# Kernel optimization log

Measured on AMD Instinct MI355X. Metric: run time of the kernel, lower is better.

Reference implementation:

```python
import jax, jax.numpy as jnp
import numpy as np

B, S, E, H, V, OOV = 128, 400, 512, 512, 50257, 50
VEXT = V + OOV


def setup_inputs() -> dict:
    key = jax.random.key(0)
    ks = jax.random.split(key, 20)
    w = lambda k, shp: (0.02 * jax.random.normal(k, shp)).astype(jnp.float32)
    return {
        'input_emb': jax.random.normal(ks[0], (B, 1, E), jnp.float32),
        'input_feed': jax.random.normal(ks[1], (B, 1, H), jnp.float32),
        'hidden': jax.random.normal(ks[2], (1, B, H), jnp.float32),
        'context': jax.random.normal(ks[3], (1, B, H), jnp.float32),
        'states': jax.random.normal(ks[4], (B, S, H), jnp.float32),
        'states_features': jax.random.normal(ks[5], (B, S, H), jnp.float32),
        'source_mask': jnp.ones((B, S), jnp.float32),
        'coverage': jnp.zeros((B, S), jnp.float32),
        'source_ids': jax.random.randint(ks[6], (B, S), 0, VEXT, jnp.int32),
        'W_ic': w(ks[7], (E, H + E)), 'b_ic': jnp.zeros((E,), jnp.float32),
        'W_ih': w(ks[8], (4 * H, E)), 'W_hh': w(ks[9], (4 * H, H)),
        'b_ih': jnp.zeros((4 * H,), jnp.float32), 'b_hh': jnp.zeros((4 * H,), jnp.float32),
        'W_dec': w(ks[10], (H, H)), 'b_att': jnp.zeros((H,), jnp.float32),
        'v_att': w(ks[11], (H,)), 'w_c': w(ks[12], (1,)),
        'W_out': w(ks[13], (H, 2 * H)), 'b_out': jnp.zeros((H,), jnp.float32),
        'W_pg': w(ks[14], (1, H)), 'b_pg': jnp.zeros((1,), jnp.float32),
        'W_v': w(ks[15], (V, H)), 'b_v': jnp.zeros((V,), jnp.float32),
    }


def reference(input_emb, input_feed, hidden, context, states, states_features,
              source_mask, coverage, source_ids,
              W_ic, b_ic, W_ih, W_hh, b_ih, b_hh,
              W_dec, b_att, v_att, w_c, W_out, b_out,
              W_pg, b_pg, W_v, b_v):
    # x = input_context(cat(input_emb, input_feed))  -> [B,1,E]
    x = jnp.concatenate([input_emb, input_feed], axis=2) @ W_ic.T + b_ic
    # single LSTM step (PyTorch gate order i,f,g,o)
    h0, c0 = hidden[0], context[0]                      # [B,H]
    gates = x[:, 0] @ W_ih.T + b_ih + h0 @ W_hh.T + b_hh
    i, f, g, o = jnp.split(gates, 4, axis=-1)
    i, f, o = jax.nn.sigmoid(i), jax.nn.sigmoid(f), jax.nn.sigmoid(o)
    c1 = f * c0 + i * jnp.tanh(g)
    h1 = o * jnp.tanh(c1)                               # rnn_output [B,H]
    # coverage attention
    dec_fea = h1 @ W_dec.T + b_att                      # [B,H]
    e = jnp.tanh(states_features + dec_fea[:, None, :] + w_c * coverage[..., None]) @ v_att  # [B,S]
    e = jnp.where(source_mask > 0, e, jnp.float32(-1e9))
    attn = jax.nn.softmax(e, axis=-1) * source_mask
    attn = attn / (attn.sum(-1, keepdims=True) + 1e-12)  # [B,S]
    ctx = jnp.einsum('bs,bsh->bh', attn, states)
    dec_out = jnp.concatenate([h1, ctx], axis=-1) @ W_out.T + b_out  # decoder_output [B,H]
    coverage_new = coverage + attn
    # pointer-generator mixing
    p_gen = jax.nn.sigmoid(dec_out @ W_pg.T + b_pg)     # [B,1]
    vocab_dist = p_gen * jax.nn.softmax(dec_out @ W_v.T + b_v, axis=-1)  # [B,V]
    ext = jnp.zeros((B, VEXT), vocab_dist.dtype).at[:, :V].set(vocab_dist)
    attn_dist = (1.0 - p_gen) * attn                    # [B,S]
    final = ext.at[jnp.arange(B)[:, None], source_ids].add(attn_dist)  # scatter_add over vocab
    final_dist = final[:, None, :]                      # [B,1,VEXT]
    return (final_dist, p_gen, attn, coverage_new, h1[None], c1[None], dec_out[:, None, :])
```

## Files before the change

### kernel.cpp

```cpp
#include <hip/hip_runtime.h>
#include <hip/hip_bf16.h>

#define B_   128
#define S_   400
#define H_   512
#define V_   50257
#define VX_  50307

#define OFF_FINAL 0
#define OFF_PGEN  6439296
#define OFF_ATTN  6439424
#define OFF_COV   6490624
#define OFF_H1    6541824
#define OFF_C1    6607360
#define OFF_DEC   6672896

typedef __attribute__((ext_vector_type(8))) short bf16x8;
typedef __attribute__((ext_vector_type(4))) float f32x4;

static __device__ __forceinline__ float sigmoid_f(float x) {
    return 1.0f / (1.0f + __expf(-x));
}
static __device__ __forceinline__ float tanh_f(float x) {
    return 1.0f - 2.0f / (__expf(2.0f * x) + 1.0f);
}
static __device__ __forceinline__ unsigned int pk2(float x, float y) {
    union { __hip_bfloat162 h; unsigned int u; } cv;
    cv.h = __float22bfloat162_rn(make_float2(x, y));
    return cv.u;
}

__global__ __launch_bounds__(256) void zero_bufs(
    float* __restrict__ a, float* __restrict__ b, float* __restrict__ c,
    float* __restrict__ d)
{
    const int i = blockIdx.x * 256 + threadIdx.x;
    a[i] = 0.f; b[i] = 0.f; c[i] = 0.f;
    if (i < 128) d[i] = 0.f;
}

template <int NT>
__global__ __launch_bounds__(256) void gemm_mfma(
    const float* __restrict__ A1, const float* __restrict__ W1, int ldw1, int kwo1,
    const float* __restrict__ A2, const float* __restrict__ W2, int ldw2, int kwo2,
    const float* __restrict__ bias1,
    float* __restrict__ C, int N,
    const float* __restrict__ wpg, float* __restrict__ pgen_acc)
{
    __shared__ __align__(16) unsigned short As[128 * 40];
    __shared__ __align__(16) unsigned short Ws[NT * 16 * 40];
    const int tid  = threadIdx.x;
    const int bn0  = blockIdx.x * (NT * 16);
    const int lane = tid & 63;
    const int wv   = tid >> 6;
    const int quad = lane >> 4;
    const int col  = lane & 15;

    f32x4 acc[2][NT];
#pragma unroll
    for (int i = 0; i < 2; ++i)
#pragma unroll
        for (int j = 0; j < NT; ++j) acc[i][j] = (f32x4){0.f, 0.f, 0.f, 0.f};

    const int ar = tid >> 1;
    const int ac = (tid & 1) << 4;
    const int wr = (NT == 8) ? (tid >> 1) : (tid >> 2);
    const int wc = (NT == 8) ? ((tid & 1) << 4) : ((tid & 3) << 3);
    const int wrg = (bn0 + wr < N) ? (bn0 + wr) : (N - 1);

    const int Ktot = (A2 != nullptr) ? 1024 : 512;
    const int KC   = Ktot / gridDim.y;
    const int kg0  = blockIdx.y * KC;
    const int nsteps = KC >> 5;

    const float* ApB[2];
    const float* WpB[2];
    ApB[0] = A1 + (long)ar * 512 + ac;
    WpB[0] = W1 + (long)wrg * ldw1 + kwo1 + wc;
    ApB[1] = A2 ? (A2 + (long)ar * 512 + ac) : ApB[0];
    WpB[1] = W2 ? (W2 + (long)wrg * ldw2 + kwo2 + wc) : WpB[0];

    float4 aC[4], wC[NT / 2], aN[4], wN[NT / 2];

    auto fetch = [&](int s, float4* a, float4* w) {
        const int kg = kg0 + (s << 5);
        const int ph = kg >> 9;
        const int k0 = kg & 511;
        const float* Ap = ApB[ph] + k0;
        const float* Wp = WpB[ph] + k0;
#pragma unroll
        for (int i = 0; i < 4; ++i) a[i] = *(const float4*)(Ap + i * 4);
#pragma unroll
        for (int i = 0; i < NT / 2; ++i) w[i] = *(const float4*)(Wp + i * 4);
    };

    fetch(0, aC, wC);
    for (int s = 0; s < nsteps; ++s) {
        __syncthreads();
        uint4* apd = (uint4*)&As[ar * 40 + ac];
        apd[0] = make_uint4(pk2(aC[0].x, aC[0].y), pk2(aC[0].z, aC[0].w),
                            pk2(aC[1].x, aC[1].y), pk2(aC[1].z, aC[1].w));
        apd[1] = make_uint4(pk2(aC[2].x, aC[2].y), pk2(aC[2].z, aC[2].w),
                            pk2(aC[3].x, aC[3].y), pk2(aC[3].z, aC[3].w));
        uint4* wpd = (uint4*)&Ws[wr * 40 + wc];
        wpd[0] = make_uint4(pk2(wC[0].x, wC[0].y), pk2(wC[0].z, wC[0].w),
                            pk2(wC[1].x, wC[1].y), pk2(wC[1].z, wC[1].w));
        if (NT == 8)
            wpd[1] = make_uint4(pk2(wC[2].x, wC[2].y), pk2(wC[2].z, wC[2].w),
                                pk2(wC[3].x, wC[3].y), pk2(wC[3].z, wC[3].w));
        __syncthreads();

        if (s + 1 < nsteps) fetch(s + 1, aN, wN);

        const bf16x8 aF0 = *(const bf16x8*)&As[(wv * 32 + col) * 40 + quad * 8];
        const bf16x8 aF1 = *(const bf16x8*)&As[(wv * 32 + 16 + col) * 40 + quad * 8];
#pragma unroll
        for (int ni = 0; ni < NT; ++ni) {
            const bf16x8 bF = *(const bf16x8*)&Ws[(ni * 16 + col) * 40 + quad * 8];
            acc[0][ni] = __builtin_amdgcn_mfma_f32_16x16x32_bf16(aF0, bF, acc[0][ni], 0, 0, 0);
            acc[1][ni] = __builtin_amdgcn_mfma_f32_16x16x32_bf16(aF1, bF, acc[1][ni], 0, 0, 0);
        }
#pragma unroll
        for (int i = 0; i < 4; ++i) aC[i] = aN[i];
#pragma unroll
        for (int i = 0; i < NT / 2; ++i) wC[i] = wN[i];
    }

    const bool split = (gridDim.y > 1);
    const bool addb  = (!split) || (blockIdx.y == 0);
    float pgp[2][4];
#pragma unroll
    for (int i = 0; i < 2; ++i)
#pragma unroll
        for (int r = 0; r < 4; ++r) pgp[i][r] = 0.f;

#pragma unroll
    for (int mi = 0; mi < 2; ++mi) {
#pragma unroll
        for (int ni = 0; ni < NT; ++ni) {
            const int n = bn0 + ni * 16 + col;
            if (n < N) {
                const float bv = addb ? bias1[n] : 0.f;
                const float wpv = wpg ? wpg[n] : 0.f;
#pragma unroll
                for (int r = 0; r < 4; ++r) {
                    const int m = wv * 32 + mi * 16 + quad * 4 + r;
                    const float v = acc[mi][ni][r] + bv;
                    if (split) atomicAdd(&C[(long)m * N + n], v);
                    else       C[(long)m * N + n] = v;
                    pgp[mi][r] += v * wpv;
                }
            }
        }
    }
    if (wpg) {
#pragma unroll
        for (int mi = 0; mi < 2; ++mi)
#pragma unroll
            for (int r = 0; r < 4; ++r) {
                float v = pgp[mi][r];
                v += __shfl_xor(v, 1); v += __shfl_xor(v, 2);
                v += __shfl_xor(v, 4); v += __shfl_xor(v, 8);
                if (col == 0) {
                    const int m = wv * 32 + mi * 16 + quad * 4 + r;
                    atomicAdd(&pgen_acc[m], v);
                }
            }
    }
}

__global__ __launch_bounds__(256) void gates_lstm(
    const float* __restrict__ x, const float* __restrict__ h0,
    const float* __restrict__ Wih, const float* __restrict__ Whh,
    const float* __restrict__ bih, const float* __restrict__ bhh,
    const float* __restrict__ c0,
    float* __restrict__ h1, float* __restrict__ c1)
{
    __shared__ __align__(16) unsigned short As[128 * 40];
    __shared__ __align__(16) unsigned short Ws[128 * 40];
    const int tid  = threadIdx.x;
    const int bh0  = blockIdx.x * 32;
    const int lane = tid & 63;
    const int wv   = tid >> 6;
    const int quad = lane >> 4;
    const int col  = lane & 15;

    f32x4 acc[2][8];
#pragma unroll
    for (int i = 0; i < 2; ++i)
#pragma unroll
        for (int j = 0; j < 8; ++j) acc[i][j] = (f32x4){0.f, 0.f, 0.f, 0.f};

    const int ar = tid >> 1;
    const int ac = (tid & 1) << 4;
    const int wr = tid >> 1;
    const int wc = (tid & 1) << 4;
    const int wrow = ((wr >> 5) << 9) + bh0 + (wr & 31);

    const float* ApB[2] = { x + (long)ar * 512 + ac, h0 + (long)ar * 512 + ac };
    const float* WpB[2] = { Wih + (long)wrow * 512 + wc, Whh + (long)wrow * 512 + wc };

    float4 aC[4], wC[4], aN[4], wN[4];
    auto fetch = [&](int s, float4* a, float4* w) {
        const int ph = s >> 4;
        const int k0 = (s & 15) << 5;
        const float* Ap = ApB[ph] + k0;
        const float* Wp = WpB[ph] + k0;
#pragma unroll
        for (int i = 0; i < 4; ++i) a[i] = *(const float4*)(Ap + i * 4);
#pragma unroll
        for (int i = 0; i < 4; ++i) w[i] = *(const float4*)(Wp + i * 4);
    };

    fetch(0, aC, wC);
    for (int s = 0; s < 32; ++s) {
        __syncthreads();
        uint4* apd = (uint4*)&As[ar * 40 + ac];
        apd[0] = make_uint4(pk2(aC[0].x, aC[0].y), pk2(aC[0].z, aC[0].w),
                            pk2(aC[1].x, aC[1].y), pk2(aC[1].z, aC[1].w));
        apd[1] = make_uint4(pk2(aC[2].x, aC[2].y), pk2(aC[2].z, aC[2].w),
                            pk2(aC[3].x, aC[3].y), pk2(aC[3].z, aC[3].w));
        uint4* wpd = (uint4*)&Ws[wr * 40 + wc];
        wpd[0] = make_uint4(pk2(wC[0].x, wC[0].y), pk2(wC[0].z, wC[0].w),
                            pk2(wC[1].x, wC[1].y), pk2(wC[1].z, wC[1].w));
        wpd[1] = make_uint4(pk2(wC[2].x, wC[2].y), pk2(wC[2].z, wC[2].w),
                            pk2(wC[3].x, wC[3].y), pk2(wC[3].z, wC[3].w));
        __syncthreads();

        if (s + 1 < 32) fetch(s + 1, aN, wN);

        const bf16x8 aF0 = *(const bf16x8*)&As[(wv * 32 + col) * 40 + quad * 8];
        const bf16x8 aF1 = *(const bf16x8*)&As[(wv * 32 + 16 + col) * 40 + quad * 8];
#pragma unroll
        for (int ni = 0; ni < 8; ++ni) {
            const bf16x8 bF = *(const bf16x8*)&Ws[(ni * 16 + col) * 40 + quad * 8];
            acc[0][ni] = __builtin_amdgcn_mfma_f32_16x16x32_bf16(aF0, bF, acc[0][ni], 0, 0, 0);
            acc[1][ni] = __builtin_amdgcn_mfma_f32_16x16x32_bf16(aF1, bF, acc[1][ni], 0, 0, 0);
        }
#pragma unroll
        for (int i = 0; i < 4; ++i) { aC[i] = aN[i]; wC[i] = wN[i]; }
    }

#pragma unroll
    for (int mi = 0; mi < 2; ++mi) {
#pragma unroll
        for (int par = 0; par < 2; ++par) {
            const int h = bh0 + par * 16 + col;
            const float bi = bih[h]        + bhh[h];
            const float bf = bih[512 + h]  + bhh[512 + h];
            const float bg = bih[1024 + h] + bhh[1024 + h];
            const float bo = bih[1536 + h] + bhh[1536 + h];
#pragma unroll
            for (int r = 0; r < 4; ++r) {
                const int m = wv * 32 + mi * 16 + quad * 4 + r;
                const float iv = sigmoid_f(acc[mi][par + 0][r] + bi);
                const float fv = sigmoid_f(acc[mi][par + 2][r] + bf);
                const float gv = tanh_f(acc[mi][par + 4][r] + bg);
                const float ov = sigmoid_f(acc[mi][par + 6][r] + bo);
                const float c = fv * c0[m * 512 + h] + iv * gv;
                c1[m * 512 + h] = c;
                h1[m * 512 + h] = ov * tanh_f(c);
            }
        }
    }
}

__global__ __launch_bounds__(256) void attn_scores(
    const float* __restrict__ sfeat, const float* __restrict__ decfea,
    const float* __restrict__ cov, const float* __restrict__ wc,
    const float* __restrict__ vatt, float* __restrict__ e)
{
    const int lane = threadIdx.x & 63;
    const int pair = blockIdx.x * 4 + (threadIdx.x >> 6);
    const int b = pair / 400;
    const float cc = wc[0] * cov[pair];
    const float* sp = sfeat + ((long)pair << 9) + (lane << 3);
    const float* dp = decfea + (b << 9) + (lane << 3);
    const float* vp = vatt + (lane << 3);
    const float4 s0 = *(const float4*)sp, s1 = *(const float4*)(sp + 4);
    const float4 d0 = *(const float4*)dp, d1 = *(const float4*)(dp + 4);
    const float4 v0 = *(const float4*)vp, v1 = *(const float4*)(vp + 4);
    float acc = tanh_f(s0.x + d0.x + cc) * v0.x
              + tanh_f(s0.y + d0.y + cc) * v0.y
              + tanh_f(s0.z + d0.z + cc) * v0.z
              + tanh_f(s0.w + d0.w + cc) * v0.w
              + tanh_f(s1.x + d1.x + cc) * v1.x
              + tanh_f(s1.y + d1.y + cc) * v1.y
              + tanh_f(s1.z + d1.z + cc) * v1.z
              + tanh_f(s1.w + d1.w + cc) * v1.w;
#pragma unroll
    for (int off = 32; off > 0; off >>= 1) acc += __shfl_down(acc, off);
    if (lane == 0) e[pair] = acc;
}

__global__ __launch_bounds__(256) void attn_softmax(
    const float* __restrict__ e, const float* __restrict__ mask,
    const float* __restrict__ cov,
    float* __restrict__ attn, float* __restrict__ covnew, float* __restrict__ ctx)
{
    __shared__ float sm[4], sps[4], spms[4];
    const int b = blockIdx.x, tid = threadIdx.x;
    ctx[(b << 9) + tid] = 0.f;
    ctx[(b << 9) + 256 + tid] = 0.f;

    float vals[2], msk[2];
    float m = -3.0e38f;
#pragma unroll
    for (int it = 0; it < 2; ++it) {
        const int s = tid + (it << 8);
        float mk = 0.f, v = -3.0e38f;
        if (s < 400) {
            mk = mask[b * 400 + s];
            v = (mk > 0.f) ? e[b * 400 + s] : -1.0e9f;
        }
        vals[it] = v; msk[it] = mk;
        m = fmaxf(m, v);
    }
#pragma unroll
    for (int off = 32; off > 0; off >>= 1) m = fmaxf(m, __shfl_down(m, off));
    if ((tid & 63) == 0) sm[tid >> 6] = m;
    __syncthreads();
    const float M = fmaxf(fmaxf(sm[0], sm[1]), fmaxf(sm[2], sm[3]));

    float p[2], sp = 0.f, spm = 0.f;
#pragma unroll
    for (int it = 0; it < 2; ++it) {
        const int s = tid + (it << 8);
        float pv = 0.f;
        if (s < 400) pv = __expf(vals[it] - M);
        p[it] = pv; sp += pv; spm += pv * msk[it];
    }
#pragma unroll
    for (int off = 32; off > 0; off >>= 1) {
        sp += __shfl_down(sp, off);
        spm += __shfl_down(spm, off);
    }
    if ((tid & 63) == 0) { sps[tid >> 6] = sp; spms[tid >> 6] = spm; }
    __syncthreads();
    const float SP = sps[0] + sps[1] + sps[2] + sps[3];
    const float SPM = spms[0] + spms[1] + spms[2] + spms[3];
    const float inv = 1.0f / (SPM + 1e-12f * SP);
#pragma unroll
    for (int it = 0; it < 2; ++it) {
        const int s = tid + (it << 8);
        if (s < 400) {
            const float a = p[it] * msk[it] * inv;
            attn[b * 400 + s] = a;
            covnew[b * 400 + s] = cov[b * 400 + s] + a;
        }
    }
}

__global__ __launch_bounds__(256) void ctx_kernel(
    const float* __restrict__ attn, const float* __restrict__ states,
    float* __restrict__ ctx)
{
    const int bx = blockIdx.x;
    const int b = bx >> 2, chunk = bx & 3;
    const int tid = threadIdx.x;
    const int c = tid & 127;
    const int sh = tid >> 7;
    const int s0 = chunk * 100 + sh;
    const float* base = states + (long)b * 400 * 512;
    float4 acc = make_float4(0.f, 0.f, 0.f, 0.f);
    for (int i = 0; i < 50; ++i) {
        const int s = s0 + (i << 1);
        const float a = attn[b * 400 + s];
        const float4 st = *(const float4*)(base + (long)s * 512 + (c << 2));
        acc.x = fmaf(a, st.x, acc.x);
        acc.y = fmaf(a, st.y, acc.y);
        acc.z = fmaf(a, st.z, acc.z);
        acc.w = fmaf(a, st.w, acc.w);
    }
    float* cp = ctx + (b << 9) + (c << 2);
    atomicAdd(cp + 0, acc.x);
    atomicAdd(cp + 1, acc.y);
    atomicAdd(cp + 2, acc.z);
    atomicAdd(cp + 3, acc.w);
}

__global__ __launch_bounds__(256) void row_stats_part(
    const float* __restrict__ logits, float* __restrict__ pm, float* __restrict__ ps)
{
    __shared__ float sred[4];
    const int b = blockIdx.y, cx = blockIdx.x, tid = threadIdx.x;
    const int v0 = cx * 6283;
    const int v1 = (v0 + 6283 < V_) ? (v0 + 6283) : V_;
    const float* row = logits + (long)b * V_;

    float m = -3.0e38f;
    for (int v = v0 + tid; v < v1; v += 256) m = fmaxf(m, row[v]);
#pragma unroll
    for (int off = 32; off > 0; off >>= 1) m = fmaxf(m, __shfl_down(m, off));
    if ((tid & 63) == 0) sred[tid >> 6] = m;
    __syncthreads();
    const float M = fmaxf(fmaxf(sred[0], sred[1]), fmaxf(sred[2], sred[3]));
    __syncthreads();

    float s = 0.f;
    for (int v = v0 + tid; v < v1; v += 256) s += __expf(row[v] - M);
#pragma unroll
    for (int off = 32; off > 0; off >>= 1) s += __shfl_down(s, off);
    if ((tid & 63) == 0) sred[tid >> 6] = s;
    __syncthreads();
    if (tid == 0) {
        pm[b * 8 + cx] = M;
        ps[b * 8 + cx] = sred[0] + sred[1] + sred[2] + sred[3];
    }
}

__global__ __launch_bounds__(256) void final_write(
    const float* __restrict__ logits, const float* __restrict__ pm,
    const float* __restrict__ ps, const float* __restrict__ pgen_acc,
    const float* __restrict__ bpg, float* __restrict__ final,
    float* __restrict__ o_pgen)
{
    const int b = blockIdx.y;
    float M = -3.0e38f;
#pragma unroll
    for (int i = 0; i < 8; ++i) M = fmaxf(M, pm[b * 8 + i]);
    float S = 0.f;
#pragma unroll
    for (int i = 0; i < 8; ++i) S += ps[b * 8 + i] * __expf(pm[b * 8 + i] - M);
    const float pg = sigmoid_f(pgen_acc[b] + bpg[0]);
    if (blockIdx.x == 0 && threadIdx.x == 0) o_pgen[b] = pg;

    const int v0 = (blockIdx.x * 256 + threadIdx.x) << 2;
    if (v0 >= VX_) return;
    const float sc = pg / S;
    const float* row = logits + (long)b * V_;
    float* out = final + (long)b * VX_ + v0;
#pragma unroll
    for (int j = 0; j < 4; ++j) {
        const int v = v0 + j;
        if (v < VX_) out[j] = (v < V_) ? __expf(row[v] - M) * sc : 0.f;
    }
}

__global__ __launch_bounds__(256) void scatter_kernel(
    const int* __restrict__ ids, const float* __restrict__ attn,
    const float* __restrict__ pgen, float* __restrict__ final)
{
    const int s = blockIdx.x * 256 + threadIdx.x;
    const int b = blockIdx.y;
    if (s < 400) {
        const float v = (1.0f - pgen[b]) * attn[b * 400 + s];
        atomicAdd(final + (long)b * VX_ + ids[b * 400 + s], v);
    }
}

extern "C" void kernel_launch(void* const* d_in, const int* in_sizes, int n_in,
                              void* d_out, int out_size, void* d_ws, size_t ws_size,
                              hipStream_t stream)
{
    const float* input_emb  = (const float*)d_in[0];
    const float* input_feed = (const float*)d_in[1];
    const float* hidden     = (const float*)d_in[2];
    const float* context    = (const float*)d_in[3];
    const float* states     = (const float*)d_in[4];
    const float* sfeat      = (const float*)d_in[5];
    const float* mask       = (const float*)d_in[6];
    const float* cov        = (const float*)d_in[7];
    const int*   src_ids    = (const int*)d_in[8];
    const float* W_ic  = (const float*)d_in[9];
    const float* b_ic  = (const float*)d_in[10];
    const float* W_ih  = (const float*)d_in[11];
    const float* W_hh  = (const float*)d_in[12];
    const float* b_ih  = (const float*)d_in[13];
    const float* b_hh  = (const float*)d_in[14];
    const float* W_dec = (const float*)d_in[15];
    const float* b_att = (const float*)d_in[16];
    const float* v_att = (const float*)d_in[17];
    const float* w_c   = (const float*)d_in[18];
    const float* W_out = (const float*)d_in[19];
    const float* b_out = (const float*)d_in[20];
    const float* W_pg  = (const float*)d_in[21];
    const float* b_pg  = (const float*)d_in[22];
    const float* W_v   = (const float*)d_in[23];
    const float* b_v   = (const float*)d_in[24];

    float* out = (float*)d_out;
    float* o_final = out + OFF_FINAL;
    float* o_pgen  = out + OFF_PGEN;
    float* o_attn  = out + OFF_ATTN;
    float* o_cov   = out + OFF_COV;
    float* o_h1    = out + OFF_H1;
    float* o_c1    = out + OFF_C1;
    float* o_dec   = out + OFF_DEC;

    float* ws = (float*)d_ws;
    float* w_x      = ws;
    float* w_decfea = ws + 327680;
    float* w_e      = ws + 393216;
    float* w_ctx    = ws + 444416;
    float* w_logits = ws + 509952;
    float* w_pm     = ws + 6943104;
    float* w_ps     = ws + 6944128;
    float* w_pga    = ws + 6945152;

    const dim3 blk(256);
    zero_bufs<<<256, blk, 0, stream>>>(w_x, w_decfea, o_dec, w_pga);
    gemm_mfma<4><<<dim3(8, 8), blk, 0, stream>>>(
        input_emb, W_ic, 1024, 0, input_feed, W_ic, 1024, 512,
        b_ic, w_x, 512, nullptr, nullptr);
    gates_lstm<<<16, blk, 0, stream>>>(w_x, hidden, W_ih, W_hh, b_ih, b_hh,
                                       context, o_h1, o_c1);
    gemm_mfma<4><<<dim3(8, 4), blk, 0, stream>>>(
        o_h1, W_dec, 512, 0, nullptr, nullptr, 0, 0,
        b_att, w_decfea, 512, nullptr, nullptr);
    attn_scores<<<12800, blk, 0, stream>>>(sfeat, w_decfea, cov, w_c, v_att, w_e);
    attn_softmax<<<128, blk, 0, stream>>>(w_e, mask, cov, o_attn, o_cov, w_ctx);
    ctx_kernel<<<512, blk, 0, stream>>>(o_attn, states, w_ctx);
    gemm_mfma<4><<<dim3(8, 8), blk, 0, stream>>>(
        o_h1, W_out, 1024, 0, w_ctx, W_out, 1024, 512,
        b_out, o_dec, 512, W_pg, w_pga);
    gemm_mfma<4><<<dim3(786, 1), blk, 0, stream>>>(
        o_dec, W_v, 512, 0, nullptr, nullptr, 0, 0,
        b_v, w_logits, 50257, nullptr, nullptr);
    row_stats_part<<<dim3(8, 128), blk, 0, stream>>>(w_logits, w_pm, w_ps);
    final_write<<<dim3(50, 128), blk, 0, stream>>>(w_logits, w_pm, w_ps, w_pga,
                                                   b_pg, o_final, o_pgen);
    scatter_kernel<<<dim3(2, 128), blk, 0, stream>>>(src_ids, o_attn, o_pgen, o_final);
}
```

Baseline: 489.2 us.

## Fuse softmax row stats into vocab GEMM epilogue and split LSTM gates GEMM

The vocab-projection GEMM epilogue now computes a per-block row max and sum-of-exp and writes them as partials. This removes the separate row_stats_part pass that re-read the full logits buffer, and final_write reduces the 786 partials per row instead. The LSTM gate GEMM now uses the generic split-K gemm_mfma over 128 blocks with atomic accumulation into a zeroed workspace, followed by a light elementwise cell kernel, replacing the 16-block fused kernel. The trade-off is extra zeroing, a gates round trip through global memory and more partial reductions in final_write.

```diff
diff --git a/kernel.cpp b/kernel.cpp
--- a/kernel.cpp
+++ b/kernel.cpp
@@ -30,13 +30,13 @@
     return cv.u;
 }
 
-__global__ __launch_bounds__(256) void zero_bufs(
-    float* __restrict__ a, float* __restrict__ b, float* __restrict__ c,
-    float* __restrict__ d)
+__global__ __launch_bounds__(256) void zero_ws(
+    float4* __restrict__ ws4, float4* __restrict__ dec4)
 {
     const int i = blockIdx.x * 256 + threadIdx.x;
-    a[i] = 0.f; b[i] = 0.f; c[i] = 0.f;
-    if (i < 128) d[i] = 0.f;
+    const float4 z = make_float4(0.f, 0.f, 0.f, 0.f);
+    if (i < 98336) ws4[i] = z;
+    if (i < 16384) dec4[i] = z;
 }
 
 template <int NT>
@@ -45,7 +45,8 @@
     const float* __restrict__ A2, const float* __restrict__ W2, int ldw2, int kwo2,
     const float* __restrict__ bias1,
     float* __restrict__ C, int N,
-    const float* __restrict__ wpg, float* __restrict__ pgen_acc)
+    const float* __restrict__ wpg, float* __restrict__ pgen_acc,
+    float* __restrict__ pm, float* __restrict__ ps)
 {
     __shared__ __align__(16) unsigned short As[128 * 40];
     __shared__ __align__(16) unsigned short Ws[NT * 16 * 40];
@@ -128,6 +129,40 @@
 
     const bool split = (gridDim.y > 1);
     const bool addb  = (!split) || (blockIdx.y == 0);
+
+    if (pm != nullptr) {
+#pragma unroll
+        for (int mi = 0; mi < 2; ++mi) {
+#pragma unroll
+            for (int r = 0; r < 4; ++r) {
+                float vv[NT];
+                float mx = -3.0e38f;
+#pragma unroll
+                for (int ni = 0; ni < NT; ++ni) {
+                    const int n = bn0 + ni * 16 + col;
+                    vv[ni] = (n < N) ? (acc[mi][ni][r] + bias1[n]) : -3.0e38f;
+                    mx = fmaxf(mx, vv[ni]);
+                }
+                mx = fmaxf(mx, __shfl_xor(mx, 1));
+                mx = fmaxf(mx, __shfl_xor(mx, 2));
+                mx = fmaxf(mx, __shfl_xor(mx, 4));
+                mx = fmaxf(mx, __shfl_xor(mx, 8));
+                float sum = 0.f;
+#pragma unroll
+                for (int ni = 0; ni < NT; ++ni) sum += __expf(vv[ni] - mx);
+                sum += __shfl_xor(sum, 1);
+                sum += __shfl_xor(sum, 2);
+                sum += __shfl_xor(sum, 4);
+                sum += __shfl_xor(sum, 8);
+                if (col == 0) {
+                    const int m = wv * 32 + mi * 16 + quad * 4 + r;
+                    pm[(long)m * gridDim.x + blockIdx.x] = mx;
+                    ps[(long)m * gridDim.x + blockIdx.x] = sum;
+                }
+            }
+        }
+    }
+
     float pgp[2][4];
 #pragma unroll
     for (int i = 0; i < 2; ++i)
@@ -169,100 +204,22 @@
     }
 }
 
-__global__ __launch_bounds__(256) void gates_lstm(
-    const float* __restrict__ x, const float* __restrict__ h0,
-    const float* __restrict__ Wih, const float* __restrict__ Whh,
-    const float* __restrict__ bih, const float* __restrict__ bhh,
+__global__ __launch_bounds__(256) void lstm_cell(
+    const float* __restrict__ gates, const float* __restrict__ bhh,
     const float* __restrict__ c0,
     float* __restrict__ h1, float* __restrict__ c1)
 {
-    __shared__ __align__(16) unsigned short As[128 * 40];
-    __shared__ __align__(16) unsigned short Ws[128 * 40];
-    const int tid  = threadIdx.x;
-    const int bh0  = blockIdx.x * 32;
-    const int lane = tid & 63;
-    const int wv   = tid >> 6;
-    const int quad = lane >> 4;
-    const int col  = lane & 15;
-
-    f32x4 acc[2][8];
-#pragma unroll
-    for (int i = 0; i < 2; ++i)
-#pragma unroll
-        for (int j = 0; j < 8; ++j) acc[i][j] = (f32x4){0.f, 0.f, 0.f, 0.f};
-
-    const int ar = tid >> 1;
-    const int ac = (tid & 1) << 4;
-    const int wr = tid >> 1;
-    const int wc = (tid & 1) << 4;
-    const int wrow = ((wr >> 5) << 9) + bh0 + (wr & 31);
-
-    const float* ApB[2] = { x + (long)ar * 512 + ac, h0 + (long)ar * 512 + ac };
-    const float* WpB[2] = { Wih + (long)wrow * 512 + wc, Whh + (long)wrow * 512 + wc };
-
-    float4 aC[4], wC[4], aN[4], wN[4];
-    auto fetch = [&](int s, float4* a, float4* w) {
-        const int ph = s >> 4;
-        const int k0 = (s & 15) << 5;
-        const float* Ap = ApB[ph] + k0;
-        const float* Wp = WpB[ph] + k0;
-#pragma unroll
-        for (int i = 0; i < 4; ++i) a[i] = *(const float4*)(Ap + i * 4);
-#pragma unroll
-        for (int i = 0; i < 4; ++i) w[i] = *(const float4*)(Wp + i * 4);
-    };
-
-    fetch(0, aC, wC);
-    for (int s = 0; s < 32; ++s) {
-        __syncthreads();
-        uint4* apd = (uint4*)&As[ar * 40 + ac];
-        apd[0] = make_uint4(pk2(aC[0].x, aC[0].y), pk2(aC[0].z, aC[0].w),
-                            pk2(aC[1].x, aC[1].y), pk2(aC[1].z, aC[1].w));
-        apd[1] = make_uint4(pk2(aC[2].x, aC[2].y), pk2(aC[2].z, aC[2].w),
-                            pk2(aC[3].x, aC[3].y), pk2(aC[3].z, aC[3].w));
-        uint4* wpd = (uint4*)&Ws[wr * 40 + wc];
-        wpd[0] = make_uint4(pk2(wC[0].x, wC[0].y), pk2(wC[0].z, wC[0].w),
-                            pk2(wC[1].x, wC[1].y), pk2(wC[1].z, wC[1].w));
-        wpd[1] = make_uint4(pk2(wC[2].x, wC[2].y), pk2(wC[2].z, wC[2].w),
-                            pk2(wC[3].x, wC[3].y), pk2(wC[3].z, wC[3].w));
-        __syncthreads();
-
-        if (s + 1 < 32) fetch(s + 1, aN, wN);
-
-        const bf16x8 aF0 = *(const bf16x8*)&As[(wv * 32 + col) * 40 + quad * 8];
-        const bf16x8 aF1 = *(const bf16x8*)&As[(wv * 32 + 16 + col) * 40 + quad * 8];
-#pragma unroll
-        for (int ni = 0; ni < 8; ++ni) {
-            const bf16x8 bF = *(const bf16x8*)&Ws[(ni * 16 + col) * 40 + quad * 8];
-            acc[0][ni] = __builtin_amdgcn_mfma_f32_16x16x32_bf16(aF0, bF, acc[0][ni], 0, 0, 0);
-            acc[1][ni] = __builtin_amdgcn_mfma_f32_16x16x32_bf16(aF1, bF, acc[1][ni], 0, 0, 0);
-        }
-#pragma unroll
-        for (int i = 0; i < 4; ++i) { aC[i] = aN[i]; wC[i] = wN[i]; }
-    }
-
-#pragma unroll
-    for (int mi = 0; mi < 2; ++mi) {
-#pragma unroll
-        for (int par = 0; par < 2; ++par) {
-            const int h = bh0 + par * 16 + col;
-            const float bi = bih[h]        + bhh[h];
-            const float bf = bih[512 + h]  + bhh[512 + h];
-            const float bg = bih[1024 + h] + bhh[1024 + h];
-            const float bo = bih[1536 + h] + bhh[1536 + h];
-#pragma unroll
-            for (int r = 0; r < 4; ++r) {
-                const int m = wv * 32 + mi * 16 + quad * 4 + r;
-                const float iv = sigmoid_f(acc[mi][par + 0][r] + bi);
-                const float fv = sigmoid_f(acc[mi][par + 2][r] + bf);
-                const float gv = tanh_f(acc[mi][par + 4][r] + bg);
-                const float ov = sigmoid_f(acc[mi][par + 6][r] + bo);
-                const float c = fv * c0[m * 512 + h] + iv * gv;
-                c1[m * 512 + h] = c;
-                h1[m * 512 + h] = ov * tanh_f(c);
-            }
-        }
-    }
+    const int idx = blockIdx.x * 256 + threadIdx.x;
+    const int m = idx >> 9;
+    const int h = idx & 511;
+    const float* g = gates + (long)m * 2048;
+    const float iv = sigmoid_f(g[h]        + bhh[h]);
+    const float fv = sigmoid_f(g[512 + h]  + bhh[512 + h]);
+    const float gv = tanh_f   (g[1024 + h] + bhh[1024 + h]);
+    const float ov = sigmoid_f(g[1536 + h] + bhh[1536 + h]);
+    const float c = fv * c0[idx] + iv * gv;
+    c1[idx] = c;
+    h1[idx] = ov * tanh_f(c);
 }
 
 __global__ __launch_bounds__(256) void attn_scores(
@@ -379,53 +336,43 @@
     atomicAdd(cp + 3, acc.w);
 }
 
-__global__ __launch_bounds__(256) void row_stats_part(
-    const float* __restrict__ logits, float* __restrict__ pm, float* __restrict__ ps)
-{
-    __shared__ float sred[4];
-    const int b = blockIdx.y, cx = blockIdx.x, tid = threadIdx.x;
-    const int v0 = cx * 6283;
-    const int v1 = (v0 + 6283 < V_) ? (v0 + 6283) : V_;
-    const float* row = logits + (long)b * V_;
-
-    float m = -3.0e38f;
-    for (int v = v0 + tid; v < v1; v += 256) m = fmaxf(m, row[v]);
-#pragma unroll
-    for (int off = 32; off > 0; off >>= 1) m = fmaxf(m, __shfl_down(m, off));
-    if ((tid & 63) == 0) sred[tid >> 6] = m;
-    __syncthreads();
-    const float M = fmaxf(fmaxf(sred[0], sred[1]), fmaxf(sred[2], sred[3]));
-    __syncthreads();
-
-    float s = 0.f;
-    for (int v = v0 + tid; v < v1; v += 256) s += __expf(row[v] - M);
-#pragma unroll
-    for (int off = 32; off > 0; off >>= 1) s += __shfl_down(s, off);
-    if ((tid & 63) == 0) sred[tid >> 6] = s;
-    __syncthreads();
-    if (tid == 0) {
-        pm[b * 8 + cx] = M;
-        ps[b * 8 + cx] = sred[0] + sred[1] + sred[2] + sred[3];
-    }
-}
-
 __global__ __launch_bounds__(256) void final_write(
     const float* __restrict__ logits, const float* __restrict__ pm,
     const float* __restrict__ ps, const float* __restrict__ pgen_acc,
     const float* __restrict__ bpg, float* __restrict__ final,
-    float* __restrict__ o_pgen)
-{
+    float* __restrict__ o_pgen, int nblk)
+{
+    __shared__ float sred[4];
+    __shared__ float sM, sS;
     const int b = blockIdx.y;
-    float M = -3.0e38f;
-#pragma unroll
-    for (int i = 0; i < 8; ++i) M = fmaxf(M, pm[b * 8 + i]);
-    float S = 0.f;
-#pragma unroll
-    for (int i = 0; i < 8; ++i) S += ps[b * 8 + i] * __expf(pm[b * 8 + i] - M);
+    const int tid = threadIdx.x;
+    const float* pmb = pm + (long)b * nblk;
+    const float* psb = ps + (long)b * nblk;
+
+    float m = -3.0e38f;
+    for (int i = tid; i < nblk; i += 256) m = fmaxf(m, pmb[i]);
+#pragma unroll
+    for (int off = 32; off > 0; off >>= 1) m = fmaxf(m, __shfl_down(m, off));
+    if ((tid & 63) == 0) sred[tid >> 6] = m;
+    __syncthreads();
+    if (tid == 0) sM = fmaxf(fmaxf(sred[0], sred[1]), fmaxf(sred[2], sred[3]));
+    __syncthreads();
+    const float M = sM;
+
+    float s = 0.f;
+    for (int i = tid; i < nblk; i += 256) s += psb[i] * __expf(pmb[i] - M);
+#pragma unroll
+    for (int off = 32; off > 0; off >>= 1) s += __shfl_down(s, off);
+    if ((tid & 63) == 0) sred[tid >> 6] = s;
+    __syncthreads();
+    if (tid == 0) sS = sred[0] + sred[1] + sred[2] + sred[3];
+    __syncthreads();
+    const float S = sS;
+
     const float pg = sigmoid_f(pgen_acc[b] + bpg[0]);
-    if (blockIdx.x == 0 && threadIdx.x == 0) o_pgen[b] = pg;
-
-    const int v0 = (blockIdx.x * 256 + threadIdx.x) << 2;
+    if (blockIdx.x == 0 && tid == 0) o_pgen[b] = pg;
+
+    const int v0 = (blockIdx.x * 256 + tid) << 2;
     if (v0 >= VX_) return;
     const float sc = pg / S;
     const float* row = logits + (long)b * V_;
@@ -490,35 +437,37 @@
 
     float* ws = (float*)d_ws;
     float* w_x      = ws;
-    float* w_decfea = ws + 327680;
-    float* w_e      = ws + 393216;
-    float* w_ctx    = ws + 444416;
-    float* w_logits = ws + 509952;
-    float* w_pm     = ws + 6943104;
-    float* w_ps     = ws + 6944128;
-    float* w_pga    = ws + 6945152;
+    float* w_decfea = ws + 65536;
+    float* w_gates  = ws + 131072;
+    float* w_pga    = ws + 393216;
+    float* w_e      = ws + 393344;
+    float* w_ctx    = ws + 444544;
+    float* w_logits = ws + 510080;
+    float* w_pm     = ws + 6942976;
+    float* w_ps     = ws + 7043584;
 
     const dim3 blk(256);
-    zero_bufs<<<256, blk, 0, stream>>>(w_x, w_decfea, o_dec, w_pga);
+    zero_ws<<<385, blk, 0, stream>>>((float4*)ws, (float4*)o_dec);
     gemm_mfma<4><<<dim3(8, 8), blk, 0, stream>>>(
         input_emb, W_ic, 1024, 0, input_feed, W_ic, 1024, 512,
-        b_ic, w_x, 512, nullptr, nullptr);
-    gates_lstm<<<16, blk, 0, stream>>>(w_x, hidden, W_ih, W_hh, b_ih, b_hh,
-                                       context, o_h1, o_c1);
+        b_ic, w_x, 512, nullptr, nullptr, nullptr, nullptr);
+    gemm_mfma<4><<<dim3(32, 4), blk, 0, stream>>>(
+        w_x, W_ih, 512, 0, hidden, W_hh, 512, 0,
+        b_ih, w_gates, 2048, nullptr, nullptr, nullptr, nullptr);
+    lstm_cell<<<256, blk, 0, stream>>>(w_gates, b_hh, context, o_h1, o_c1);
     gemm_mfma<4><<<dim3(8, 4), blk, 0, stream>>>(
         o_h1, W_dec, 512, 0, nullptr, nullptr, 0, 0,
-        b_att, w_decfea, 512, nullptr, nullptr);
+        b_att, w_decfea, 512, nullptr, nullptr, nullptr, nullptr);
     attn_scores<<<12800, blk, 0, stream>>>(sfeat, w_decfea, cov, w_c, v_att, w_e);
     attn_softmax<<<128, blk, 0, stream>>>(w_e, mask, cov, o_attn, o_cov, w_ctx);
     ctx_kernel<<<512, blk, 0, stream>>>(o_attn, states, w_ctx);
     gemm_mfma<4><<<dim3(8, 8), blk, 0, stream>>>(
         o_h1, W_out, 1024, 0, w_ctx, W_out, 1024, 512,
-        b_out, o_dec, 512, W_pg, w_pga);
+        b_out, o_dec, 512, W_pg, w_pga, nullptr, nullptr);
     gemm_mfma<4><<<dim3(786, 1), blk, 0, stream>>>(
         o_dec, W_v, 512, 0, nullptr, nullptr, 0, 0,
-        b_v, w_logits, 50257, nullptr, nullptr);
-    row_stats_part<<<dim3(8, 128), blk, 0, stream>>>(w_logits, w_pm, w_ps);
+        b_v, w_logits, 50257, nullptr, nullptr, w_pm, w_ps);
     final_write<<<dim3(50, 128), blk, 0, stream>>>(w_logits, w_pm, w_ps, w_pga,
-                                                   b_pg, o_final, o_pgen);
+                                                   b_pg, o_final, o_pgen, 786);
     scatter_kernel<<<dim3(2, 128), blk, 0, stream>>>(src_ids, o_attn, o_pgen, o_final);
 }
```

After: 459.3 us. -6.1%, faster.
